# Optimization experiments

Measured on AMD Instinct MI355X. Metric: run time of the kernel, lower is better.

## Reference

```python
import jax, jax.numpy as jnp
import numpy as np

D_IN = 768
D_SAE = 768 * 16  # expansion_factor = 16
K = 64
BATCH = 8192


def setup_inputs() -> dict:
    key = jax.random.key(0)
    k1, k2, k3 = jax.random.split(key, 3)
    x = jax.random.normal(k1, (BATCH, D_IN), dtype=jnp.float32)
    # Kaiming-uniform-ish encoder init (exact init values don't matter for correctness)
    bound = (6.0 / D_IN) ** 0.5
    W_enc = jax.random.uniform(k2, (D_IN, D_SAE), dtype=jnp.float32, minval=-bound, maxval=bound)
    b_enc = jnp.zeros((D_SAE,), dtype=jnp.float32)
    W_dec = jax.random.normal(k3, (D_SAE, D_IN), dtype=jnp.float32) * (1.0 / D_IN ** 0.5)
    # unit-norm decoder rows (per the module's normalize_decoder_weights)
    W_dec = W_dec / (jnp.linalg.norm(W_dec, axis=1, keepdims=True) + 1e-8)
    b_dec = jnp.zeros((D_IN,), dtype=jnp.float32)
    return {"x": x, "W_enc": W_enc, "b_enc": b_enc, "W_dec": W_dec, "b_dec": b_dec}


def reference(x, W_enc, b_enc, W_dec, b_dec):
    # encode: center, dense matmul, ReLU
    pre_acts = jax.nn.relu((x - b_dec) @ W_enc + b_enc)  # [B, d_sae]
    # top-k selection per row, scatter back into dense sparse_acts
    topk_vals, topk_idx = jax.lax.top_k(pre_acts, K)  # [B, K]
    rows = jnp.arange(pre_acts.shape[0])[:, None]  # [B, 1]
    sparse_acts = jnp.zeros_like(pre_acts).at[rows, topk_idx].set(topk_vals)
    # decode: dense matmul + bias
    reconstruction = sparse_acts @ W_dec + b_dec  # [B, d_in]
    return (reconstruction, sparse_acts)
```

## Files before the change

### kernel.cpp

```cpp
#include <hip/hip_runtime.h>
#include <hip/hip_fp16.h>
#include <stdint.h>

#define D_IN   768
#define D_SAE  12288
#define BATCH  8192
#define K_TOP  64
#define CAND_MAX 256

typedef _Float16 f16;
typedef _Float16 v8h __attribute__((ext_vector_type(8)));
typedef float v4f __attribute__((ext_vector_type(4)));

__device__ inline void async16(const void* g, void* l) {
    __builtin_amdgcn_global_load_lds(
        (const __attribute__((address_space(1))) unsigned int*)g,
        (__attribute__((address_space(3))) unsigned int*)l, 16, 0, 0);
}

__global__ __launch_bounds__(256) void k_convert_x(
    const float* __restrict__ x, const float* __restrict__ b_dec,
    f16* __restrict__ xhi)
{
    int i4 = (blockIdx.x * 256 + threadIdx.x) * 4;
    float4 v = *(const float4*)(x + i4);
    int col = i4 % D_IN;
    float vv[4] = { v.x - b_dec[col], v.y - b_dec[col + 1],
                    v.z - b_dec[col + 2], v.w - b_dec[col + 3] };
    union { short4 s; f16 h[4]; } H;
#pragma unroll
    for (int u = 0; u < 4; ++u) H.h[u] = (f16)vv[u];
    *(short4*)(xhi + i4) = H.s;
}

__global__ __launch_bounds__(256) void k_convert_wt(
    const float* __restrict__ W, f16* __restrict__ whiT, f16* __restrict__ wloT)
{
    __shared__ float tile[32][33];
    const int n0 = blockIdx.x * 32;
    const int k0 = blockIdx.y * 32;
    const int c = threadIdx.x & 31;
    const int rr = threadIdx.x >> 5;
#pragma unroll
    for (int s = 0; s < 4; ++s) {
        int r = s * 8 + rr;
        tile[r][c] = W[(size_t)(k0 + r) * D_SAE + n0 + c];
    }
    __syncthreads();
#pragma unroll
    for (int s = 0; s < 4; ++s) {
        int r2 = s * 8 + rr;
        float v = tile[c][r2];
        f16 hi = (f16)v;
        f16 lo = (f16)(v - (float)hi);
        whiT[(size_t)(n0 + r2) * D_IN + k0 + c] = hi;
        wloT[(size_t)(n0 + r2) * D_IN + k0 + c] = lo;
    }
}

__global__ __launch_bounds__(256) void k_convert_wd(
    const float* __restrict__ W, f16* __restrict__ Wh)
{
    int i4 = (blockIdx.x * 256 + threadIdx.x) * 4;
    float4 v = *(const float4*)(W + i4);
    union { short4 s; f16 h[4]; } H;
    H.h[0] = (f16)v.x; H.h[1] = (f16)v.y; H.h[2] = (f16)v.z; H.h[3] = (f16)v.w;
    *(short4*)(Wh + i4) = H.s;
}

__global__ __launch_bounds__(256) void k_gemm_f16(
    const f16* __restrict__ A,
    const f16* __restrict__ Bt,
    const float* __restrict__ b_enc,
    f16* __restrict__ outap)
{
    __shared__ f16 Asm[2][128 * 32];
    __shared__ f16 Bsm[2][128 * 32];
    const int tid  = threadIdx.x;
    const int wave = tid >> 6;
    const int lane = tid & 63;
    const int bn = blockIdx.x * 128;
    const int bm = blockIdx.y * 128;

    const int r16  = lane >> 2;
    const int kc8  = (lane & 3) * 8;
    const int mrow = lane & 15;
    const int quad = lane >> 4;
    const int wm = (wave & 1) * 64;
    const int wn = (wave >> 1) * 64;

    v4f acc[4][4] = {};

    const f16* gA = A  + (size_t)(bm + wave * 32 + r16) * D_IN + kc8;
    const f16* gB = Bt + (size_t)(bn + wave * 32 + r16) * D_IN + kc8;
    f16* lA0  = &Asm[0][(wave * 32) * 32];
    f16* lA0b = &Asm[0][(wave * 32 + 16) * 32];
    f16* lB0  = &Bsm[0][(wave * 32) * 32];
    f16* lB0b = &Bsm[0][(wave * 32 + 16) * 32];
    f16* lA1  = &Asm[1][(wave * 32) * 32];
    f16* lA1b = &Asm[1][(wave * 32 + 16) * 32];
    f16* lB1  = &Bsm[1][(wave * 32) * 32];
    f16* lB1b = &Bsm[1][(wave * 32 + 16) * 32];

    for (int k0 = 0; k0 < D_IN; k0 += 64) {
        __syncthreads();
        async16(gA + k0,               lA0);
        async16(gA + k0 + 16 * D_IN,   lA0b);
        async16(gB + k0,               lB0);
        async16(gB + k0 + 16 * D_IN,   lB0b);
        async16(gA + k0 + 32,              lA1);
        async16(gA + k0 + 32 + 16 * D_IN,  lA1b);
        async16(gB + k0 + 32,              lB1);
        async16(gB + k0 + 32 + 16 * D_IN,  lB1b);
        __syncthreads();

#pragma unroll
        for (int s = 0; s < 2; ++s) {
            v8h af[4], bf[4];
#pragma unroll
            for (int i = 0; i < 4; ++i)
                af[i] = *(const v8h*)&Asm[s][(wm + i * 16 + mrow) * 32 + quad * 8];
#pragma unroll
            for (int j = 0; j < 4; ++j)
                bf[j] = *(const v8h*)&Bsm[s][(wn + j * 16 + mrow) * 32 + quad * 8];
#pragma unroll
            for (int i = 0; i < 4; ++i)
#pragma unroll
                for (int j = 0; j < 4; ++j)
                    acc[i][j] = __builtin_amdgcn_mfma_f32_16x16x32_f16(af[i], bf[j], acc[i][j], 0, 0, 0);
        }
    }

#pragma unroll
    for (int i = 0; i < 4; ++i) {
#pragma unroll
        for (int r = 0; r < 4; ++r) {
            int grow = bm + wm + i * 16 + quad * 4 + r;
            f16* op = outap + (size_t)grow * (2 * D_SAE) + bn + wn;
#pragma unroll
            for (int j = 0; j < 4; ++j) {
                int c = j * 16 + mrow;
                float val = acc[i][j][r] + b_enc[bn + wn + c];
                __builtin_nontemporal_store((f16)(val > 0.f ? val : 0.f), op + c);
            }
        }
    }

    {
        float* zbase = (float*)outap;
        const int r = tid >> 1;
        const int half = (tid & 1) * 32;
        float* zp = zbase + (size_t)(bm + r) * D_SAE + (D_SAE / 2)
                  + blockIdx.x * 64 + half;
        v4f z = {0.f, 0.f, 0.f, 0.f};
#pragma unroll
        for (int q = 0; q < 8; ++q)
            __builtin_nontemporal_store(z, (v4f*)(zp + q * 4));
    }
}

__device__ __forceinline__ unsigned suffix_scan_256(unsigned h, int t, unsigned* wtot, unsigned* tot_out) {
    const int lane = t & 63;
    const int w = t >> 6;
    unsigned s = h;
#pragma unroll
    for (int off = 1; off < 64; off <<= 1) {
        unsigned o = __shfl_down(s, off);
        if (lane + off < 64) s += o;
    }
    if (lane == 0) wtot[w] = s;
    __syncthreads();
    unsigned suf = s;
    unsigned tot = 0;
#pragma unroll
    for (int w2 = 0; w2 < 4; ++w2) {
        tot += wtot[w2];
        if (w2 > w) suf += wtot[w2];
    }
    *tot_out = tot;
    return suf;
}

__global__ __launch_bounds__(256) void k_topk2(
    float* __restrict__ sparse,
    const float* __restrict__ x,
    const f16* __restrict__ WhiT, const f16* __restrict__ WloT,
    const float* __restrict__ b_enc,
    const f16* __restrict__ Wdh,
    const float* __restrict__ b_dec,
    float* __restrict__ recon)
{
    const int row = blockIdx.x;
    const int t = threadIdx.x;
    const int lane = t & 63;
    float* rp = sparse + (size_t)row * D_SAE;
    const f16* ap = (const f16*)rp;

    v8h av[6];
#pragma unroll
    for (int j = 0; j < 6; ++j)
        av[j] = __builtin_nontemporal_load((const v8h*)(ap + ((size_t)j * 256 + t) * 8));

    __shared__ unsigned hist[256];
    __shared__ unsigned wtot[4];
    __shared__ float sh_cutoff;
    __shared__ int sh_ncand;
    __shared__ int   cand_i[CAND_MAX];
    __shared__ float cand_v[CAND_MAX];
    __shared__ float kept_v[K_TOP];
    __shared__ int   kept_i[K_TOP];
    __shared__ float xr[D_IN];

    const float margin = 0.05f;

    hist[t] = 0;
    if (t == 0) sh_ncand = 0;
    for (int k = t; k < D_IN; k += 256)
        xr[k] = x[(size_t)row * D_IN + k] - b_dec[k];
    __syncthreads();

#pragma unroll
    for (int j = 0; j < 6; ++j)
#pragma unroll
        for (int u = 0; u < 8; ++u) {
            float x0 = (float)av[j][u];
            if (x0 >= 2.0f) {
                int b = (int)((x0 - 2.0f) * 32.0f); if (b > 255) b = 255;
                atomicAdd(&hist[b], 1u);
            }
        }
    __syncthreads();
    unsigned h0 = hist[t];
    unsigned tot0;
    unsigned suf0 = suffix_scan_256(h0, t, wtot, &tot0);
    if (tot0 >= K_TOP) {
        if (suf0 >= K_TOP && suf0 - h0 < K_TOP)
            sh_cutoff = fmaxf(2.0f + (float)t * (1.0f / 32.0f) - margin, 1e-30f);
    }
    __syncthreads();
    if (tot0 < K_TOP) {
        hist[t] = 0;
        __syncthreads();
#pragma unroll
        for (int j = 0; j < 6; ++j)
#pragma unroll
            for (int u = 0; u < 8; ++u) {
                float x0 = (float)av[j][u];
                if (x0 >= 0.25f) {
                    int b = (int)(x0 * 32.0f); if (b > 255) b = 255;
                    atomicAdd(&hist[b], 1u);
                }
            }
        __syncthreads();
        unsigned h1 = hist[t];
        unsigned tot1;
        unsigned suf1 = suffix_scan_256(h1, t, wtot, &tot1);
        if (tot1 >= K_TOP) {
            if (suf1 >= K_TOP && suf1 - h1 < K_TOP)
                sh_cutoff = fmaxf((float)t * (1.0f / 32.0f) - margin, 1e-30f);
        }
        __syncthreads();
        if (tot1 < K_TOP) {
            hist[t] = 0;
            __syncthreads();
#pragma unroll
            for (int j = 0; j < 6; ++j)
#pragma unroll
                for (int u = 0; u < 8; ++u) {
                    float x0 = (float)av[j][u];
                    if (x0 > 0.0f && x0 < 0.25f) {
                        int b = (int)(x0 * 1024.0f); if (b > 255) b = 255;
                        atomicAdd(&hist[b], 1u);
                    }
                }
            __syncthreads();
            unsigned h2 = hist[t];
            unsigned tot2;
            unsigned suf2 = suffix_scan_256(h2, t, wtot, &tot2);
            unsigned need = K_TOP - tot1;
            if (tot2 >= need) {
                if (suf2 >= need && suf2 - h2 < need)
                    sh_cutoff = fmaxf((float)t * (1.0f / 1024.0f) - margin, 1e-30f);
            } else {
                if (t == 0) sh_cutoff = 1e-30f;
            }
        }
    }
    __syncthreads();
    const float cutoff = sh_cutoff;

#pragma unroll
    for (int j = 0; j < 6; ++j)
#pragma unroll
        for (int u = 0; u < 8; ++u) {
            float x0 = (float)av[j][u];
            bool pass = (x0 >= cutoff);
            unsigned long long m = __ballot(pass);
            if (m != 0ull) {
                int leader = (int)__builtin_ctzll(m);
                int cnt = (int)__builtin_popcountll(m);
                int base0 = 0;
                if (lane == leader) base0 = atomicAdd(&sh_ncand, cnt);
                base0 = __shfl(base0, leader);
                if (pass) {
                    int pos = base0 + (int)__builtin_popcountll(m & ((1ull << lane) - 1ull));
                    if (pos < CAND_MAX) { cand_i[pos] = (j * 256 + t) * 8 + u; cand_v[pos] = x0; }
                }
            }
        }
    __syncthreads();
    int ncand = sh_ncand; if (ncand > CAND_MAX) ncand = CAND_MAX;

    for (int c = t; c < ncand; c += 256) {
        const f16* wh = WhiT + (size_t)cand_i[c] * D_IN;
        const f16* wl = WloT + (size_t)cand_i[c] * D_IN;
        float acc = 0.f;
        for (int k = 0; k < D_IN; k += 8) {
            v8h hv = *(const v8h*)(wh + k);
            v8h lv = *(const v8h*)(wl + k);
#pragma unroll
            for (int u = 0; u < 8; ++u)
                acc += xr[k + u] * ((float)hv[u] + (float)lv[u]);
        }
        acc += b_enc[cand_i[c]];
        cand_v[c] = acc > 0.f ? acc : 0.f;
    }
    __syncthreads();

    for (int c = t; c < ncand; c += 256) {
        float vc = cand_v[c]; int ic = cand_i[c];
        int r = 0;
        for (int m = 0; m < ncand; ++m) {
            float vm = cand_v[m];
            r += (vm > vc || (vm == vc && cand_i[m] < ic)) ? 1 : 0;
        }
        if (r < K_TOP) { kept_v[r] = vc; kept_i[r] = ic; }
    }
    __syncthreads();
    int nk = ncand < K_TOP ? ncand : K_TOP;

#pragma unroll
    for (int j = 0; j < 6; ++j) {
        v4f z = {0.f, 0.f, 0.f, 0.f};
        __builtin_nontemporal_store(z, (v4f*)(rp + ((size_t)j * 256 + t) * 4));
    }
    __syncthreads();
    if (t < nk) rp[kept_i[t]] = kept_v[t];

    float r0 = b_dec[t], r1 = b_dec[t + 256], r2 = b_dec[t + 512];
#pragma unroll 4
    for (int m = 0; m < nk; ++m) {
        float val = kept_v[m];
        const f16* wr = Wdh + (size_t)kept_i[m] * D_IN;
        r0 += val * (float)wr[t];
        r1 += val * (float)wr[t + 256];
        r2 += val * (float)wr[t + 512];
    }
    float* rc = recon + (size_t)row * D_IN;
    __builtin_nontemporal_store(r0, rc + t);
    __builtin_nontemporal_store(r1, rc + t + 256);
    __builtin_nontemporal_store(r2, rc + t + 512);
}

extern "C" void kernel_launch(void* const* d_in, const int* in_sizes, int n_in,
                              void* d_out, int out_size, void* d_ws, size_t ws_size,
                              hipStream_t stream) {
    const float* x     = (const float*)d_in[0];
    const float* W_enc = (const float*)d_in[1];
    const float* b_enc = (const float*)d_in[2];
    const float* W_dec = (const float*)d_in[3];
    const float* b_dec = (const float*)d_in[4];
    float* out    = (float*)d_out;
    float* recon  = out;
    float* sparse = out + (size_t)BATCH * D_IN;

    const size_t xplane = (size_t)BATCH * D_IN;
    const size_t wplane = (size_t)D_SAE * D_IN;
    f16* xhi    = (f16*)d_ws;
    f16* whiT   = xhi + xplane;
    f16* wloT   = whiT + wplane;
    f16* wdh    = wloT + wplane;

    k_convert_x<<<xplane / 1024, 256, 0, stream>>>(x, b_dec, xhi);
    k_convert_wt<<<dim3(D_SAE / 32, D_IN / 32), 256, 0, stream>>>(W_enc, whiT, wloT);
    k_convert_wd<<<wplane / 1024, 256, 0, stream>>>(W_dec, wdh);
    k_gemm_f16<<<dim3(D_SAE / 128, BATCH / 128), 256, 0, stream>>>(xhi, whiT, b_enc, (f16*)sparse);
    k_topk2<<<BATCH, 256, 0, stream>>>(sparse, x, whiT, wloT, b_enc, wdh, b_dec, recon);
}
```

Measured before the change: 1.362 ms.

## Stage GEMM epilogue through LDS for coalesced 16-byte stores, move zeroing to topk

The GEMM epilogue used to write scattered 2-byte f16 values straight to global memory and also zero the upper half of each output row. It now applies bias and ReLU into a padded LDS tile that reuses the A/B staging buffers, then writes full 16-byte vectors per thread. The zeroing of the second half of the row moves to the later top-k kernel, whose zero loop is doubled to cover the whole row. This adds two barriers and an LDS round trip in exchange for coalesced wide stores, and puts more write work in the top-k kernel.

```diff
diff --git a/kernel.cpp b/kernel.cpp
--- a/kernel.cpp
+++ b/kernel.cpp
@@ -74,8 +74,10 @@
     const float* __restrict__ b_enc,
     f16* __restrict__ outap)
 {
-    __shared__ f16 Asm[2][128 * 32];
-    __shared__ f16 Bsm[2][128 * 32];
+    __shared__ union {
+        struct { f16 A[2][128 * 32]; f16 B[2][128 * 32]; } ab;
+        f16 C[128 * 136];
+    } sm;
     const int tid  = threadIdx.x;
     const int wave = tid >> 6;
     const int lane = tid & 63;
@@ -93,14 +95,14 @@
 
     const f16* gA = A  + (size_t)(bm + wave * 32 + r16) * D_IN + kc8;
     const f16* gB = Bt + (size_t)(bn + wave * 32 + r16) * D_IN + kc8;
-    f16* lA0  = &Asm[0][(wave * 32) * 32];
-    f16* lA0b = &Asm[0][(wave * 32 + 16) * 32];
-    f16* lB0  = &Bsm[0][(wave * 32) * 32];
-    f16* lB0b = &Bsm[0][(wave * 32 + 16) * 32];
-    f16* lA1  = &Asm[1][(wave * 32) * 32];
-    f16* lA1b = &Asm[1][(wave * 32 + 16) * 32];
-    f16* lB1  = &Bsm[1][(wave * 32) * 32];
-    f16* lB1b = &Bsm[1][(wave * 32 + 16) * 32];
+    f16* lA0  = &sm.ab.A[0][(wave * 32) * 32];
+    f16* lA0b = &sm.ab.A[0][(wave * 32 + 16) * 32];
+    f16* lB0  = &sm.ab.B[0][(wave * 32) * 32];
+    f16* lB0b = &sm.ab.B[0][(wave * 32 + 16) * 32];
+    f16* lA1  = &sm.ab.A[1][(wave * 32) * 32];
+    f16* lA1b = &sm.ab.A[1][(wave * 32 + 16) * 32];
+    f16* lB1  = &sm.ab.B[1][(wave * 32) * 32];
+    f16* lB1b = &sm.ab.B[1][(wave * 32 + 16) * 32];
 
     for (int k0 = 0; k0 < D_IN; k0 += 64) {
         __syncthreads();
@@ -119,10 +121,10 @@
             v8h af[4], bf[4];
 #pragma unroll
             for (int i = 0; i < 4; ++i)
-                af[i] = *(const v8h*)&Asm[s][(wm + i * 16 + mrow) * 32 + quad * 8];
+                af[i] = *(const v8h*)&sm.ab.A[s][(wm + i * 16 + mrow) * 32 + quad * 8];
 #pragma unroll
             for (int j = 0; j < 4; ++j)
-                bf[j] = *(const v8h*)&Bsm[s][(wn + j * 16 + mrow) * 32 + quad * 8];
+                bf[j] = *(const v8h*)&sm.ab.B[s][(wn + j * 16 + mrow) * 32 + quad * 8];
 #pragma unroll
             for (int i = 0; i < 4; ++i)
 #pragma unroll
@@ -131,31 +133,29 @@
         }
     }
 
-#pragma unroll
-    for (int i = 0; i < 4; ++i) {
-#pragma unroll
-        for (int r = 0; r < 4; ++r) {
-            int grow = bm + wm + i * 16 + quad * 4 + r;
-            f16* op = outap + (size_t)grow * (2 * D_SAE) + bn + wn;
-#pragma unroll
-            for (int j = 0; j < 4; ++j) {
-                int c = j * 16 + mrow;
-                float val = acc[i][j][r] + b_enc[bn + wn + c];
-                __builtin_nontemporal_store((f16)(val > 0.f ? val : 0.f), op + c);
-            }
-        }
-    }
-
+    __syncthreads();
+#pragma unroll
+    for (int i = 0; i < 4; ++i)
+#pragma unroll
+        for (int j = 0; j < 4; ++j)
+#pragma unroll
+            for (int r = 0; r < 4; ++r) {
+                int lrow = wm + i * 16 + quad * 4 + r;
+                int lcol = wn + j * 16 + mrow;
+                float val = acc[i][j][r] + b_enc[bn + lcol];
+                sm.C[lrow * 136 + lcol] = (f16)(val > 0.f ? val : 0.f);
+            }
+    __syncthreads();
     {
-        float* zbase = (float*)outap;
-        const int r = tid >> 1;
-        const int half = (tid & 1) * 32;
-        float* zp = zbase + (size_t)(bm + r) * D_SAE + (D_SAE / 2)
-                  + blockIdx.x * 64 + half;
-        v4f z = {0.f, 0.f, 0.f, 0.f};
-#pragma unroll
-        for (int q = 0; q < 8; ++q)
-            __builtin_nontemporal_store(z, (v4f*)(zp + q * 4));
+        const int r0 = tid >> 4;
+        const int c8 = (tid & 15) * 8;
+#pragma unroll
+        for (int q = 0; q < 8; ++q) {
+            int lrow = r0 + q * 16;
+            v8h v = *(const v8h*)&sm.C[lrow * 136 + c8];
+            __builtin_nontemporal_store(v,
+                (v8h*)(outap + (size_t)(bm + lrow) * (2 * D_SAE) + bn + c8));
+        }
     }
 }
 
@@ -340,7 +340,7 @@
     int nk = ncand < K_TOP ? ncand : K_TOP;
 
 #pragma unroll
-    for (int j = 0; j < 6; ++j) {
+    for (int j = 0; j < 12; ++j) {
         v4f z = {0.f, 0.f, 0.f, 0.f};
         __builtin_nontemporal_store(z, (v4f*)(rp + ((size_t)j * 256 + t) * 4));
     }
```

After: 1.197 ms. -12.1%, faster.
